# Optimization experiments

Measured on AMD Instinct MI355X. Metric: run time of the kernel, lower is better.

The kernel has to match this reference:

```python
import jax, jax.numpy as jnp
import numpy as np

N = 100000      # nodes
E = 3200000     # edges
IN = 64         # in_channels
OUT = 256       # out_channels (hidden)
OSZ = 4         # output_size


def setup_inputs() -> dict:
    key = jax.random.key(0)
    ks = jax.random.split(key, 16)
    s = 0.05
    inp = {
        "x": jax.random.normal(ks[0], (N, IN), jnp.float32),
        "edge_index": jax.random.randint(ks[1], (2, E), 0, N, jnp.int64),
        # GCNConv weights for z, r, h gates: [IN, OUT] + bias [OUT]
        "Wz": jax.random.normal(ks[2], (IN, OUT), jnp.float32) * s,
        "bz": jnp.zeros((OUT,), jnp.float32),
        "Wr": jax.random.normal(ks[3], (IN, OUT), jnp.float32) * s,
        "br": jnp.zeros((OUT,), jnp.float32),
        "Wh": jax.random.normal(ks[4], (IN, OUT), jnp.float32) * s,
        "bh": jnp.zeros((OUT,), jnp.float32),
        # GRU linear layers: [2*OUT, OUT] + bias [OUT]
        "Lzw": jax.random.normal(ks[5], (2 * OUT, OUT), jnp.float32) * s,
        "Lzb": jnp.zeros((OUT,), jnp.float32),
        "Lrw": jax.random.normal(ks[6], (2 * OUT, OUT), jnp.float32) * s,
        "Lrb": jnp.zeros((OUT,), jnp.float32),
        "Lhw": jax.random.normal(ks[7], (2 * OUT, OUT), jnp.float32) * s,
        "Lhb": jnp.zeros((OUT,), jnp.float32),
        # output head
        "Wo": jax.random.normal(ks[8], (OUT, OSZ), jnp.float32) * s,
        "bo": jnp.zeros((OSZ,), jnp.float32),
    }
    return inp


def _gcn_conv(x, W, b, src, dst, n):
    # GCNConv with symmetric normalization and self-loops (fill_value=1):
    # out = D^{-1/2}(A+I)D^{-1/2} X W + b
    ones = jnp.ones_like(src, dtype=x.dtype)
    deg = jax.ops.segment_sum(ones, dst, num_segments=n) + 1.0  # +1 for self-loop
    dinv = jax.lax.rsqrt(deg)                                   # [N]
    norm = dinv[src] * dinv[dst]                                # [E]
    agg = jax.ops.segment_sum(x[src] * norm[:, None], dst, num_segments=n)
    agg = agg + x * (dinv * dinv)[:, None]                      # self-loop term
    return agg @ W + b


def reference(x, edge_index, Wz, bz, Wr, br, Wh, bh,
              Lzw, Lzb, Lrw, Lrb, Lhw, Lhb, Wo, bo):
    src, dst = edge_index[0], edge_index[1]
    n = x.shape[0]
    H = jnp.zeros((n, Wz.shape[1]), x.dtype)  # TGCN initial hidden state
    # update gate
    Z = jax.nn.sigmoid(jnp.concatenate([_gcn_conv(x, Wz, bz, src, dst, n), H], 1) @ Lzw + Lzb)
    # reset gate
    R = jax.nn.sigmoid(jnp.concatenate([_gcn_conv(x, Wr, br, src, dst, n), H], 1) @ Lrw + Lrb)
    # candidate state
    Ht = jnp.tanh(jnp.concatenate([_gcn_conv(x, Wh, bh, src, dst, n), H * R], 1) @ Lhw + Lhb)
    H = Z * H + (1.0 - Z) * Ht
    # head: ReLU -> Linear -> Softmax(dim=1)
    h = jax.nn.relu(H)
    return jax.nn.softmax(h @ Wo + bo, axis=1)
```

## Files before the change

kernel.cpp:

```cpp
#include <hip/hip_runtime.h>
#include <hip/hip_fp16.h>


#define SHIFT 7
#define NPB   128
#define BMAX  1024
#define TILE  8192
#define EPT   16
#define MBBLK 64
#define CAPB  5120

typedef __attribute__((ext_vector_type(8))) short short8;
typedef __attribute__((ext_vector_type(4))) float floatx4;

__device__ __forceinline__ ushort f2b(float f) {
    union { float f; unsigned u; } v; v.f = f;
    unsigned r = v.u + 0x7FFFu + ((v.u >> 16) & 1u);
    return (ushort)(r >> 16);
}

__device__ __forceinline__ float fastrcp(float x) {
    return __builtin_amdgcn_rcpf(x);
}

__global__ __launch_bounds__(512) void scatter_build_kernel(
    const int* __restrict__ srcs, const int* __restrict__ dsts,
    int* __restrict__ gcur, int* __restrict__ staging, int E, int B, int nT,
    const float* __restrict__ Wz, const float* __restrict__ bz,
    const float* __restrict__ Wh, const float* __restrict__ bh,
    const float* __restrict__ Lzw, const float* __restrict__ Lzb,
    const float* __restrict__ Lhw, const float* __restrict__ Lhb,
    ushort* __restrict__ Mb, float* __restrict__ cb) {
    __shared__ int cnt[BMAX];
    __shared__ int ssum[BMAX];
    __shared__ int gbase[BMAX];
    __shared__ int cur[BMAX];
    __shared__ int sorted[TILE];
    if (blockIdx.x < nT) {
        int tid = threadIdx.x;
        for (int i = tid; i < BMAX; i += 512) cnt[i] = 0;
        __syncthreads();
        int tile0 = blockIdx.x * TILE;
        int dreg[EPT];
#pragma unroll
        for (int j = 0; j < EPT; ++j) {
            int e = tile0 + j * 512 + tid;
            dreg[j] = (e < E) ? dsts[e] : -1;
            if (dreg[j] >= 0) atomicAdd(&cnt[((unsigned)dreg[j]) >> SHIFT], 1);
        }
        __syncthreads();
        {
            int i0 = tid, i1 = tid + 512;
            ssum[i0] = cnt[i0];
            ssum[i1] = cnt[i1];
            __syncthreads();
            for (int off = 1; off < BMAX; off <<= 1) {
                int t0 = (i0 >= off) ? ssum[i0 - off] : 0;
                int t1 = (i1 >= off) ? ssum[i1 - off] : 0;
                __syncthreads();
                ssum[i0] += t0;
                ssum[i1] += t1;
                __syncthreads();
            }
        }
        for (int i = tid; i < BMAX; i += 512) {
            int c = cnt[i];
            gbase[i] = (c > 0) ? atomicAdd(&gcur[i], c) : 0;
            cur[i] = ssum[i] - c;
        }
        __syncthreads();
#pragma unroll
        for (int j = 0; j < EPT; ++j) {
            int d = dreg[j];
            if (d >= 0) {
                int e = tile0 + j * 512 + tid;
                int s = srcs[e];
                int b = ((unsigned)d) >> SHIFT;
                int pos = atomicAdd(&cur[b], 1);
                sorted[pos] = ((d & (NPB - 1)) << 17) | s;
            }
        }
        __syncthreads();
        int grp = tid >> 4, l16 = tid & 15;
        for (int b = grp; b < B; b += 32) {
            int c = cnt[b];
            if (c == 0) continue;
            int lb = ssum[b] - c;
            int gb = gbase[b];
            size_t gp = (size_t)b * CAPB + gb;
            for (int j = l16; j < c; j += 16)
                if (gb + j < CAPB) staging[gp + j] = sorted[lb + j];
        }
    } else {
        int j = (blockIdx.x - nT) * 8 + (threadIdx.x >> 6);
        int k = threadIdx.x & 63;
        int which = j >> 8;
        int jj = j & 255;
        const float* W  = which ? Wh  : Wz;
        const float* bv = which ? bh  : bz;
        const float* L  = which ? Lhw : Lzw;
        const float* Lb = which ? Lhb : Lzb;
        const float4* Wr = (const float4*)(W + k * 256);
        float acc = 0.f;
        for (int t4 = 0; t4 < 64; ++t4) {
            float4 wv = Wr[t4];
            int t = t4 * 4;
            acc = fmaf(wv.x, L[(t + 0) * 256 + jj], acc);
            acc = fmaf(wv.y, L[(t + 1) * 256 + jj], acc);
            acc = fmaf(wv.z, L[(t + 2) * 256 + jj], acc);
            acc = fmaf(wv.w, L[(t + 3) * 256 + jj], acc);
        }
        Mb[j * 64 + k] = f2b(acc);
        if (k == 0) {
            float a = 0.f;
            for (int t = 0; t < 256; ++t) a = fmaf(bv[t], L[t * 256 + jj], a);
            cb[j] = a + Lb[jj];
        }
    }
}

__global__ __launch_bounds__(512) void prep_sort_kernel(
    const int* __restrict__ staging,
    const int* __restrict__ gcur,
    const float* __restrict__ x,
    int* __restrict__ deg,
    int* __restrict__ startg,
    int* __restrict__ csr,
    __half* __restrict__ xsq,
    int n, int B) {
    int b = blockIdx.x;
    int tid = threadIdx.x;
    __shared__ int   nd[NPB];
    __shared__ int   ssc[NPB];
    __shared__ int   ncur[NPB];
    __shared__ float sdinv[NPB];
    __shared__ int   csrl[CAPB];
    if (tid < NPB) nd[tid] = 0;
    __syncthreads();
    int count = gcur[b];
    if (count > CAPB) count = CAPB;
    size_t base = (size_t)b * CAPB;
    for (int i = tid; i < count; i += 512)
        atomicAdd(&nd[staging[base + i] >> 17], 1);
    __syncthreads();
    int d0 = 0;
    if (tid < NPB) { d0 = nd[tid]; ssc[tid] = d0; }
    __syncthreads();
    for (int off = 1; off < NPB; off <<= 1) {
        int t = 0;
        if (tid < NPB && tid >= off) t = ssc[tid - off];
        __syncthreads();
        if (tid < NPB) ssc[tid] += t;
        __syncthreads();
    }
    if (tid < NPB) {
        int excl = ssc[tid] - d0;
        ncur[tid] = excl;
        float dn = rsqrtf((float)d0 + 1.0f);
        sdinv[tid] = dn;
        int node = (b << SHIFT) + tid;
        if (node < n) {
            deg[node] = d0;
            startg[node] = excl;
        }
    }
    __syncthreads();
    for (int i = tid; i < count; i += 512) {
        int p = staging[base + i];
        int pos = atomicAdd(&ncur[p >> 17], 1);
        if (pos < CAPB) csrl[pos] = p & 0x1FFFF;
    }
    __syncthreads();
    for (int i = tid; i < count; i += 512)
        csr[base + i] = csrl[i];
    int nbase = b << SHIFT;
    for (int i2 = tid; i2 < NPB * 16; i2 += 512) {
        int nl = i2 >> 4;
        int g  = i2 & 15;
        int node = nbase + nl;
        if (node < n) {
            float dn = sdinv[nl];
            float4 vx = ((const float4*)x)[(size_t)node * 16 + g];
            __half2 a  = __floats2half2_rn(vx.x * dn, vx.y * dn);
            __half2 c2 = __floats2half2_rn(vx.z * dn, vx.w * dn);
            int q = g >> 2;
            size_t off = ((size_t)q * n + node) * 16 + (size_t)(g & 3) * 4;
            *(__half2*)(xsq + off)     = a;
            *(__half2*)(xsq + off + 2) = c2;
        }
    }
}

__global__ __launch_bounds__(512) void quarter_gather_kernel(
    const int* __restrict__ csr,
    const int* __restrict__ startg,
    const int* __restrict__ deg,
    const __half* __restrict__ xsq,
    ushort* __restrict__ aggb, int n, int B) {
    int blk = blockIdx.x;
    int xcd = blk & 7;
    int q   = xcd >> 1;
    int b   = ((blk >> 3) << 1) | (xcd & 1);
    if (b >= B) return;
    int tid = threadIdx.x;
    __shared__ int   sstart[NPB];
    __shared__ int   sdeg[NPB];
    __shared__ float sdinv[NPB];
    int node0 = b << SHIFT;
    if (tid < NPB) {
        int nodeid = node0 + tid;
        int dg = (nodeid < n) ? deg[nodeid] : 0;
        sdeg[tid]   = dg;
        sstart[tid] = (nodeid < n) ? startg[nodeid] : 0;
        sdinv[tid]  = rsqrtf((float)dg + 1.0f);
    }
    __syncthreads();
    const __half* xq  = xsq + (size_t)q * n * 16;
    const int* csrb   = csr + (size_t)b * CAPB;
    int wv = tid >> 6, lane = tid & 63;
    int ns = lane >> 4;
    int eg = (lane >> 1) & 7;
    int c  = lane & 1;
    for (int grp = 0; grp < 4; ++grp) {
        int nl   = (wv << 4) + (grp << 2) + ns;
        int node = node0 + nl;
        int s0 = sstart[nl];
        int d  = sdeg[nl];
        __half2 hz = __float2half2_rn(0.f);
        __half2 hacc[4] = {hz, hz, hz, hz};
        int full = d & ~7;
        for (int be = 0; be < full; be += 8) {
            int idx = csrb[s0 + be + eg];
            union { uint4 u; __half2 h[4]; } p;
            p.u = *(const uint4*)(xq + (size_t)idx * 16 + c * 8);
#pragma unroll
            for (int t = 0; t < 4; ++t) hacc[t] = __hadd2(hacc[t], p.h[t]);
        }
        if (full < d) {
            int e = full + eg;
            int idx = csrb[s0 + (e < d ? e : 0)];
            union { uint4 u; __half2 h[4]; } p;
            p.u = *(const uint4*)(xq + (size_t)idx * 16 + c * 8);
            if (e >= d) p.u = make_uint4(0u, 0u, 0u, 0u);
#pragma unroll
            for (int t = 0; t < 4; ++t) hacc[t] = __hadd2(hacc[t], p.h[t]);
        }
#pragma unroll
        for (int off = 8; off >= 2; off >>= 1) {
#pragma unroll
            for (int t = 0; t < 4; ++t) {
                union { __half2 h; int i; } u;
                u.h = hacc[t];
                u.i = __shfl_down(u.i, off);
                hacc[t] = __hadd2(hacc[t], u.h);
            }
        }
        if (eg == 0 && node < n) {
            float dn = sdinv[nl];
            union { uint4 u; __half2 h[4]; } p;
            p.u = *(const uint4*)(xq + (size_t)node * 16 + c * 8);
            uint4 o;
            unsigned* ow = (unsigned*)&o;
#pragma unroll
            for (int t = 0; t < 4; ++t) {
                float2 a = __half22float2(hacc[t]);
                float2 f = __half22float2(p.h[t]);
                float v0 = dn * fmaf(f.x, dn, a.x);
                float v1 = dn * fmaf(f.y, dn, a.y);
                ow[t] = (unsigned)f2b(v0) | ((unsigned)f2b(v1) << 16);
            }
            *(uint4*)(aggb + (size_t)node * 64 + q * 16 + c * 8) = o;
        }
    }
}

__global__ __launch_bounds__(512) void node_mfma_kernel(
    const ushort* __restrict__ aggb,
    const ushort* __restrict__ Mb,
    const float* __restrict__ cb,
    const float* __restrict__ Wo, const float* __restrict__ bo,
    float* __restrict__ out, int n) {
    int tid  = threadIdx.x;
    int w    = tid >> 6;
    int lane = tid & 63;
    int nidx = lane & 15;
    int quad = lane >> 4;
    short8 bfz[2][2], bfh[2][2];
    float cbz[2], cbh[2];
#pragma unroll
    for (int cg = 0; cg < 2; ++cg) {
        int colZ = (w << 5) + (cg << 4) + nidx;
        int colH = 256 + colZ;
#pragma unroll
        for (int s = 0; s < 2; ++s) {
            bfz[cg][s] = *(const short8*)(Mb + colZ * 64 + s * 32 + quad * 8);
            bfh[cg][s] = *(const short8*)(Mb + colH * 64 + s * 32 + quad * 8);
        }
        cbz[cg] = cb[colZ];
        cbh[cg] = cb[colH];
    }
    __shared__ float sH[32][260];
    __shared__ float sWo[4][256];
    if (tid < 256) {
#pragma unroll
        for (int o = 0; o < 4; ++o) sWo[o][tid] = Wo[tid * 4 + o];
    }
    float bo0 = bo[0], bo1 = bo[1], bo2 = bo[2], bo3 = bo[3];
    int ntiles = (n + 31) >> 5;
    for (int tile = blockIdx.x; tile < ntiles; tile += gridDim.x) {
        int node0 = tile << 5;
        int nA0 = node0 + nidx;
        int nA1 = node0 + 16 + nidx;
        if (nA0 >= n) nA0 = n - 1;
        if (nA1 >= n) nA1 = n - 1;
        const ushort* ar0 = aggb + (size_t)nA0 * 64;
        const ushort* ar1 = aggb + (size_t)nA1 * 64;
        short8 a00 = *(const short8*)(ar0 + quad * 8);
        short8 a01 = *(const short8*)(ar0 + 32 + quad * 8);
        short8 a10 = *(const short8*)(ar1 + quad * 8);
        short8 a11 = *(const short8*)(ar1 + 32 + quad * 8);
#pragma unroll
        for (int cg = 0; cg < 2; ++cg) {
            int col = (w << 5) + (cg << 4) + nidx;
#pragma unroll
            for (int grp = 0; grp < 2; ++grp) {
                short8 a0 = grp ? a10 : a00;
                short8 a1 = grp ? a11 : a01;
                floatx4 cz = {cbz[cg], cbz[cg], cbz[cg], cbz[cg]};
                cz = __builtin_amdgcn_mfma_f32_16x16x32_bf16(a0, bfz[cg][0], cz, 0, 0, 0);
                cz = __builtin_amdgcn_mfma_f32_16x16x32_bf16(a1, bfz[cg][1], cz, 0, 0, 0);
                floatx4 chh = {cbh[cg], cbh[cg], cbh[cg], cbh[cg]};
                chh = __builtin_amdgcn_mfma_f32_16x16x32_bf16(a0, bfh[cg][0], chh, 0, 0, 0);
                chh = __builtin_amdgcn_mfma_f32_16x16x32_bf16(a1, bfh[cg][1], chh, 0, 0, 0);
#pragma unroll
                for (int r = 0; r < 4; ++r) {
                    int row = (grp << 4) + (quad << 2) + r;
                    float zc = fastrcp(1.0f + __expf(cz[r]));
                    float th = 1.0f - 2.0f * fastrcp(1.0f + __expf(2.0f * chh[r]));
                    sH[row][col] = fmaxf(zc * th, 0.0f);
                }
            }
        }
        __syncthreads();
        {
            int nb = tid >> 4, g = tid & 15;
            float l0 = 0.f, l1 = 0.f, l2 = 0.f, l3 = 0.f;
#pragma unroll
            for (int ii = 0; ii < 16; ++ii) {
                int ch = g + 16 * ii;
                float hv = sH[nb][ch];
                l0 = fmaf(hv, sWo[0][ch], l0);
                l1 = fmaf(hv, sWo[1][ch], l1);
                l2 = fmaf(hv, sWo[2][ch], l2);
                l3 = fmaf(hv, sWo[3][ch], l3);
            }
#pragma unroll
            for (int off = 8; off > 0; off >>= 1) {
                l0 += __shfl_down(l0, off, 16);
                l1 += __shfl_down(l1, off, 16);
                l2 += __shfl_down(l2, off, 16);
                l3 += __shfl_down(l3, off, 16);
            }
            int node = node0 + nb;
            if (g == 0 && node < n) {
                float v0 = l0 + bo0, v1 = l1 + bo1, v2 = l2 + bo2, v3 = l3 + bo3;
                float mx = fmaxf(fmaxf(v0, v1), fmaxf(v2, v3));
                float e0 = __expf(v0 - mx), e1 = __expf(v1 - mx);
                float e2 = __expf(v2 - mx), e3 = __expf(v3 - mx);
                float inv = fastrcp(e0 + e1 + e2 + e3);
                float4 o;
                o.x = e0 * inv; o.y = e1 * inv; o.z = e2 * inv; o.w = e3 * inv;
                ((float4*)out)[node] = o;
            }
        }
        __syncthreads();
    }
}

extern "C" void kernel_launch(void* const* d_in, const int* in_sizes, int n_in,
                              void* d_out, int out_size, void* d_ws, size_t ws_size,
                              hipStream_t stream) {
    const float* x   = (const float*)d_in[0];
    const int*  eidx = (const int*)d_in[1];
    const float* Wz  = (const float*)d_in[2];
    const float* bz  = (const float*)d_in[3];
    const float* Wh  = (const float*)d_in[6];
    const float* bh  = (const float*)d_in[7];
    const float* Lzw = (const float*)d_in[8];
    const float* Lzb = (const float*)d_in[9];
    const float* Lhw = (const float*)d_in[12];
    const float* Lhb = (const float*)d_in[13];
    const float* Wo  = (const float*)d_in[14];
    const float* bo  = (const float*)d_in[15];
    float* out = (float*)d_out;

    int n = in_sizes[0] / 64;
    int E = in_sizes[1] / 2;
    const int* srcs = eidx;
    const int* dsts = eidx + E;
    int B = (n + NPB - 1) >> SHIFT;
    int nT = (E + TILE - 1) / TILE;

    size_t na = ((size_t)n + 3) & ~(size_t)3;
    size_t bucketArr = (((size_t)B * CAPB * 4) + 255) & ~(size_t)255;
    size_t aggBytes  = (((size_t)n * 64 * 2) + 255) & ~(size_t)255;

    char* ws = (char*)d_ws;
    int*   deg    = (int*)ws;    ws += na * 4;
    int*   startg = (int*)ws;    ws += na * 4;
    int*   gcur   = (int*)ws;    ws += BMAX * 4;
    int*   staging = (int*)ws;   ws += bucketArr;
    int*   csr    = (int*)ws;    ws += bucketArr;
    __half* xsq   = (__half*)ws; ws += (size_t)n * 64 * 2;
    ushort* aggb  = (ushort*)ws; ws += aggBytes;
    ushort* Mb    = (ushort*)ws; ws += 512 * 64 * 2;
    float* cb     = (float*)ws;  ws += 512 * 4;

    hipMemsetAsync(gcur, 0, BMAX * 4, stream);
    scatter_build_kernel<<<nT + MBBLK, 512, 0, stream>>>(srcs, dsts, gcur,
                                                         staging, E, B, nT,
                                                         Wz, bz, Wh, bh,
                                                         Lzw, Lzb, Lhw, Lhb,
                                                         Mb, cb);
    prep_sort_kernel<<<B, 512, 0, stream>>>(staging, gcur, x, deg, startg,
                                            csr, xsq, n, B);
    int gq = 8 * ((B + 1) / 2);
    quarter_gather_kernel<<<gq, 512, 0, stream>>>(csr, startg, deg, xsq,
                                                  aggb, n, B);
    node_mfma_kernel<<<1024, 512, 0, stream>>>(aggb, Mb, cb, Wo, bo, out, n);
}
```

Measured before the change: 280.2 us.

## Stage CSR indices in LDS and software-pipeline gather loads two deep

Each block first copies its CSR slice (CAPB ints) from global memory into shared memory with nontemporal loads, then reads neighbour indices from LDS. The gather loop is restructured so two feature loads are in flight ahead of the accumulation, which increases memory-level parallelism on the dependent index-then-feature load chain. In exchange it adds about 20KB of LDS per block, which may lower occupancy, plus an upfront copy of the whole slice even where degrees are small.

```diff
diff --git a/kernel.cpp b/kernel.cpp
--- a/kernel.cpp
+++ b/kernel.cpp
@@ -203,6 +203,7 @@
     int b   = ((blk >> 3) << 1) | (xcd & 1);
     if (b >= B) return;
     int tid = threadIdx.x;
+    __shared__ int   csrl[CAPB];
     __shared__ int   sstart[NPB];
     __shared__ int   sdeg[NPB];
     __shared__ float sdinv[NPB];
@@ -214,9 +215,13 @@
         sstart[tid] = (nodeid < n) ? startg[nodeid] : 0;
         sdinv[tid]  = rsqrtf((float)dg + 1.0f);
     }
-    __syncthreads();
-    const __half* xq  = xsq + (size_t)q * n * 16;
-    const int* csrb   = csr + (size_t)b * CAPB;
+    {
+        const int* csrb = csr + (size_t)b * CAPB;
+        for (int i = tid; i < CAPB; i += 512)
+            csrl[i] = __builtin_nontemporal_load(&csrb[i]);
+    }
+    __syncthreads();
+    const __half* xq = xsq + (size_t)q * n * 16;
     int wv = tid >> 6, lane = tid & 63;
     int ns = lane >> 4;
     int eg = (lane >> 1) & 7;
@@ -228,17 +233,39 @@
         int d  = sdeg[nl];
         __half2 hz = __float2half2_rn(0.f);
         __half2 hacc[4] = {hz, hz, hz, hz};
-        int full = d & ~7;
-        for (int be = 0; be < full; be += 8) {
-            int idx = csrb[s0 + be + eg];
-            union { uint4 u; __half2 h[4]; } p;
-            p.u = *(const uint4*)(xq + (size_t)idx * 16 + c * 8);
+        int nb8 = (d & ~7) >> 3;
+        uint4 pA, pB;
+        if (nb8 >= 1) {
+            int idx = csrl[s0 + eg];
+            pA = *(const uint4*)(xq + (size_t)idx * 16 + c * 8);
+        }
+        if (nb8 >= 2) {
+            int idx = csrl[s0 + 8 + eg];
+            pB = *(const uint4*)(xq + (size_t)idx * 16 + c * 8);
+        }
+        for (int i = 2; i < nb8; ++i) {
+            int idx = csrl[s0 + i * 8 + eg];
+            uint4 pC = *(const uint4*)(xq + (size_t)idx * 16 + c * 8);
+            union { uint4 u; __half2 h[4]; } p; p.u = pA;
 #pragma unroll
             for (int t = 0; t < 4; ++t) hacc[t] = __hadd2(hacc[t], p.h[t]);
-        }
+            pA = pB; pB = pC;
+        }
+        if (nb8 >= 2) {
+            union { uint4 u; __half2 h[4]; } p; p.u = pA;
+#pragma unroll
+            for (int t = 0; t < 4; ++t) hacc[t] = __hadd2(hacc[t], p.h[t]);
+            pA = pB;
+        }
+        if (nb8 >= 1) {
+            union { uint4 u; __half2 h[4]; } p; p.u = pA;
+#pragma unroll
+            for (int t = 0; t < 4; ++t) hacc[t] = __hadd2(hacc[t], p.h[t]);
+        }
+        int full = nb8 << 3;
         if (full < d) {
             int e = full + eg;
-            int idx = csrb[s0 + (e < d ? e : 0)];
+            int idx = csrl[s0 + (e < d ? e : 0)];
             union { uint4 u; __half2 h[4]; } p;
             p.u = *(const uint4*)(xq + (size_t)idx * 16 + c * 8);
             if (e >= d) p.u = make_uint4(0u, 0u, 0u, 0u);
```

Result: no change. 285.7 us (+1.9%).
